# Optimization experiments

Measured on AMD Instinct MI355X. Metric: run time of the kernel, lower is better.

Reference implementation:

```python
import jax, jax.numpy as jnp
import numpy as np

ORDER = 3  # truncation level; num_components = ORDER*(ORDER+1)//2 = 6 (independent weights)


def setup_inputs() -> dict:
    key = jax.random.key(0)
    k1, k2, k3 = jax.random.split(key, 3)
    B, T, D, F = 64, 4096, 128, 64
    C = ORDER * (ORDER + 1) // 2
    sequences = jax.random.normal(k1, (B, T, D), dtype=jnp.float32)
    # ls2t_uniform-style init: scaled uniform per component
    kernel = jax.random.normal(k2, (C, D, F), dtype=jnp.float32) / np.sqrt(D)
    bias = jax.random.normal(k3, (C, F), dtype=jnp.float32) * 0.01
    return {"sequences": sequences, "kernel": kernel, "bias": bias}


def _exclusive_cumsum(x, axis):
    # exclusive cumsum = inclusive cumsum minus self (avoids concat/pad allocs)
    return jnp.cumsum(x, axis=axis) - x


def reference(sequences, kernel, bias):
    # sequences: [B, T, D]; kernel: [C, D, F]; bias: [C, F]
    # M[c] = sequences @ kernel[c] + bias[c]  -> [C, B, T, F]
    M = jnp.einsum('btd,cdf->cbtf', sequences, kernel) + bias[:, None, None, :]
    # Level 1: plain sum over time of first component
    Y = [jnp.sum(M[0], axis=1)]  # [B, F]
    k = 1
    for m in range(1, ORDER):
        R = M[k]
        k += 1
        for _ in range(m):
            # iterated-sum recursion: strictly-lower-triangular (exclusive) cumsum over time
            R = M[k] * _exclusive_cumsum(R, axis=1)
            k += 1
        Y.append(jnp.sum(R, axis=1))
    return jnp.stack(Y, axis=-1)  # [B, F, ORDER]
```

## Files before the change

### kernel.cpp

```cpp
#include <hip/hip_runtime.h>
#include <hip/hip_bf16.h>


#define B_ 64
#define T_ 4096
#define D_ 128
#define F_ 64
#define TB 512
#define TGROUPS (T_ / TB)
#define CHT 16
#define NITER (TB / CHT)
#define TPB 512
#define RING 4

typedef __attribute__((ext_vector_type(8))) short short8v;
typedef __attribute__((ext_vector_type(4))) float f32x4;

__device__ __forceinline__ unsigned short bfb(float x) {
    __hip_bfloat16 h = __float2bfloat16(x);
    unsigned short u;
    __builtin_memcpy(&u, &h, 2);
    return u;
}

#define BAR() asm volatile("s_waitcnt lgkmcnt(0)\n\ts_barrier" ::: "memory")
#define VW(n) asm volatile("s_waitcnt vmcnt(" #n ")" ::: "memory")

__global__ __launch_bounds__(TPB)
void ls2t_kernel(const float* __restrict__ seq,
                 const float* __restrict__ kern,
                 const float* __restrict__ bias,
                 float* __restrict__ ws)
{
    __shared__ float slds[RING][CHT * D_];

    const int tid  = threadIdx.x;
    const int tg   = blockIdx.x;
    const int b    = blockIdx.y;
    const int lane = tid & 63;
    const int w    = tid >> 6;
    const int cg   = w >> 2;
    const int wv   = w & 3;
    const int fr   = lane & 15;
    const int lg   = lane >> 4;
    const int f    = wv * 16 + fr;

    short8v bfrag[3][4];
    float bc[3];
    #pragma unroll
    for (int cc = 0; cc < 3; ++cc) {
        const int c = cg * 3 + cc;
        bc[cc] = bias[c * F_ + f];
        #pragma unroll
        for (int ks = 0; ks < 4; ++ks) {
            const float* kp = kern + ((size_t)c * D_ + ks * 32 + lg * 8) * F_ + f;
            short8v bf;
            #pragma unroll
            for (int j = 0; j < 8; ++j) bf[j] = (short)bfb(kp[(size_t)j * F_]);
            bfrag[cc][ks] = bf;
        }
    }

    const float* sbase = seq + ((size_t)b * T_ + (size_t)tg * TB) * D_;

    const int r_lane = 2 * w + (lane >> 5);
    const int u_lane = lane & 31;
    const int gu     = (u_lane & 24) | ((u_lane ^ r_lane) & 7);
    const float* gsrc0 = sbase
        + ((size_t)((r_lane >> 2) * 128 + (r_lane & 3))) * D_ + gu * 4;

    auto issue = [&](int i, int bufi) {
        const float* src = gsrc0 + (size_t)i * 4 * D_;
        void* dst = (void*)&slds[bufi][w * 256];
        __builtin_amdgcn_global_load_lds(
            (const __attribute__((address_space(1))) void*)src,
            (__attribute__((address_space(3))) void*)dst, 16, 0, 0);
    };

    float x0 = 0.f, x1 = 0.f, x2 = 0.f, x3 = 0.f, x4 = 0.f, x5 = 0.f;

    auto compute = [&](int bufi) {
        const float* L = &slds[bufi][0];
        f32x4 acc[3];
        #pragma unroll
        for (int cc = 0; cc < 3; ++cc)
            acc[cc] = (f32x4){bc[cc], bc[cc], bc[cc], bc[cc]};

        #pragma unroll
        for (int ks = 0; ks < 4; ++ks) {
            const int u0 = ks * 8 + lg * 2;
            const int s0 = (u0 & 24) | ((u0 ^ fr) & 7);
            const int s1 = ((u0 + 1) & 24) | (((u0 + 1) ^ fr) & 7);
            float4 fa = *reinterpret_cast<const float4*>(&L[fr * 128 + s0 * 4]);
            float4 fb = *reinterpret_cast<const float4*>(&L[fr * 128 + s1 * 4]);
            uint4 pk;
            pk.x = __builtin_amdgcn_perm(__float_as_uint(fa.y),
                                         __float_as_uint(fa.x), 0x07060302u);
            pk.y = __builtin_amdgcn_perm(__float_as_uint(fa.w),
                                         __float_as_uint(fa.z), 0x07060302u);
            pk.z = __builtin_amdgcn_perm(__float_as_uint(fb.y),
                                         __float_as_uint(fb.x), 0x07060302u);
            pk.w = __builtin_amdgcn_perm(__float_as_uint(fb.w),
                                         __float_as_uint(fb.z), 0x07060302u);
            short8v a = *reinterpret_cast<short8v*>(&pk);
            #pragma unroll
            for (int cc = 0; cc < 3; ++cc)
                acc[cc] = __builtin_amdgcn_mfma_f32_16x16x32_bf16(
                    a, bfrag[cc][ks], acc[cc], 0, 0, 0);
        }

        #pragma unroll
        for (int r = 0; r < 4; ++r) {
            float p = acc[0][r], q = acc[1][r], rr = acc[2][r];
            x5 = fmaf(rr, x3, x5);
            x4 = fmaf(rr, x1, x4);
            x3 = fmaf(q,  x0, x3);
            x2 += rr;
            x1 += q;
            x0 += p;
        }
    };

    issue(0, 0); issue(1, 1); issue(2, 2);

    #pragma unroll 1
    for (int i = 0; i < NITER - 3; ++i) {
        VW(2);
        BAR();
        issue(i + 3, (i + 3) & 3);
        compute(i & 3);
    }
    VW(2); BAR(); compute(1);
    VW(1); BAR(); compute(2);
    VW(0); BAR(); compute(3);

    #pragma unroll
    for (int m = 16; m <= 32; m <<= 1) {
        float o0 = __shfl_xor(x0, m), o1 = __shfl_xor(x1, m);
        float o2 = __shfl_xor(x2, m), o3 = __shfl_xor(x3, m);
        float o4 = __shfl_xor(x4, m), o5 = __shfl_xor(x5, m);
        const bool up = (lane & m) != 0;
        float A0 = up ? o0 : x0, B0 = up ? x0 : o0;
        float A1 = up ? o1 : x1, B1 = up ? x1 : o1;
        float A2 = up ? o2 : x2, B2 = up ? x2 : o2;
        float A3 = up ? o3 : x3, B3 = up ? x3 : o3;
        float A4 = up ? o4 : x4, B4 = up ? x4 : o4;
        float A5 = up ? o5 : x5, B5 = up ? x5 : o5;
        x5 = A5 + B5 + A3 * B2 + A0 * B4;
        x4 = A4 + B4 + A1 * B2;
        x3 = A3 + B3 + A0 * B1;
        x2 = A2 + B2;
        x1 = A1 + B1;
        x0 = A0 + B0;
    }

    if (lg == 0) {
        float* wp = ws + (((size_t)b * TGROUPS + tg) * F_ + f) * 10;
        if (cg == 0) {
            wp[0] = x0; wp[1] = x1; wp[2] = x2; wp[3] = x4;
        } else {
            wp[4] = x0; wp[5] = x1; wp[6] = x2;
            wp[7] = x3; wp[8] = x4; wp[9] = x5;
        }
    }
}

struct St { float a0, s1, s2, q2, su, sv, sw, qvu, qwv, qwvu; };

__device__ __forceinline__ St mergeSt(const St& A, const St& B) {
    St r;
    r.a0   = A.a0 + B.a0;
    r.q2   = A.q2 + B.q2 + A.s1 * B.s2;
    r.s1   = A.s1 + B.s1;
    r.s2   = A.s2 + B.s2;
    r.qwvu = A.qwvu + B.qwvu + A.qvu * B.sw + A.su * B.qwv;
    r.qwv  = A.qwv + B.qwv + A.sv * B.sw;
    r.qvu  = A.qvu + B.qvu + A.su * B.sv;
    r.su   = A.su + B.su;
    r.sv   = A.sv + B.sv;
    r.sw   = A.sw + B.sw;
    return r;
}

__global__ __launch_bounds__(64)
void ls2t_fold_kernel(const float* __restrict__ ws, float* __restrict__ out)
{
    const int b = blockIdx.x;
    const int f = threadIdx.x;
    St A = {0, 0, 0, 0, 0, 0, 0, 0, 0, 0};
    #pragma unroll
    for (int g = 0; g < TGROUPS; ++g) {
        const float* rp = ws + (((size_t)b * TGROUPS + g) * F_ + f) * 10;
        St r = {rp[0], rp[1], rp[2], rp[3], rp[4],
                rp[5], rp[6], rp[7], rp[8], rp[9]};
        A = mergeSt(A, r);
    }
    float* op = out + ((size_t)b * F_ + f) * 3;
    op[0] = A.a0;
    op[1] = A.q2;
    op[2] = A.qwvu;
}

extern "C" void kernel_launch(void* const* d_in, const int* in_sizes, int n_in,
                              void* d_out, int out_size, void* d_ws, size_t ws_size,
                              hipStream_t stream) {
    const float* seq  = (const float*)d_in[0];
    const float* kern = (const float*)d_in[1];
    const float* bias = (const float*)d_in[2];
    float* out = (float*)d_out;
    float* ws  = (float*)d_ws;

    dim3 g1(TGROUPS, B_);
    ls2t_kernel<<<g1, TPB, 0, stream>>>(seq, kern, bias, ws);
    ls2t_fold_kernel<<<B_, F_, 0, stream>>>(ws, out);
}
```

Before: 43.43 us.

## Replace LDS ring pipeline with direct register double-buffered loads and split blocks

Drops the shared-memory ring filled by global_load_lds and has each lane load its MFMA A-fragment straight from global memory into registers, double-buffered across two chunks. Each component group now gets its own 256-thread block, so the grid doubles and block indices are remapped (presumably to spread work across XCDs). The intent is to remove the LDS round trip and most barriers and to raise occupancy with launch_bounds(256,3). The cost is that both component groups now read the same sequence data separately, doubling global traffic, and the register footprint grows.

```diff
diff --git a/kernel.cpp b/kernel.cpp
--- a/kernel.cpp
+++ b/kernel.cpp
@@ -8,10 +8,9 @@
 #define F_ 64
 #define TB 512
 #define TGROUPS (T_ / TB)
-#define CHT 16
-#define NITER (TB / CHT)
-#define TPB 512
-#define RING 4
+#define NITER 32
+#define TPB 256
+#define NBLK (B_ * TGROUPS * 2)
 
 typedef __attribute__((ext_vector_type(8))) short short8v;
 typedef __attribute__((ext_vector_type(4))) float f32x4;
@@ -23,24 +22,23 @@
     return u;
 }
 
-#define BAR() asm volatile("s_waitcnt lgkmcnt(0)\n\ts_barrier" ::: "memory")
 #define VW(n) asm volatile("s_waitcnt vmcnt(" #n ")" ::: "memory")
 
-__global__ __launch_bounds__(TPB)
+__global__ __launch_bounds__(TPB, 3)
 void ls2t_kernel(const float* __restrict__ seq,
                  const float* __restrict__ kern,
                  const float* __restrict__ bias,
                  float* __restrict__ ws)
 {
-    __shared__ float slds[RING][CHT * D_];
-
-    const int tid  = threadIdx.x;
-    const int tg   = blockIdx.x;
-    const int b    = blockIdx.y;
+    const int tid = threadIdx.x;
+    const int bid     = blockIdx.x;
+    const int logical = (bid & 7) * (NBLK / 8) + (bid >> 3);
+    const int cg = logical & 1;
+    const int tg = (logical >> 1) & (TGROUPS - 1);
+    const int b  = logical >> 4;
+
     const int lane = tid & 63;
-    const int w    = tid >> 6;
-    const int cg   = w >> 2;
-    const int wv   = w & 3;
+    const int wv   = tid >> 6;
     const int fr   = lane & 15;
     const int lg   = lane >> 4;
     const int f    = wv * 16 + fr;
@@ -61,26 +59,22 @@
         }
     }
 
-    const float* sbase = seq + ((size_t)b * T_ + (size_t)tg * TB) * D_;
-
-    const int r_lane = 2 * w + (lane >> 5);
-    const int u_lane = lane & 31;
-    const int gu     = (u_lane & 24) | ((u_lane ^ r_lane) & 7);
-    const float* gsrc0 = sbase
-        + ((size_t)((r_lane >> 2) * 128 + (r_lane & 3))) * D_ + gu * 4;
-
-    auto issue = [&](int i, int bufi) {
-        const float* src = gsrc0 + (size_t)i * 4 * D_;
-        void* dst = (void*)&slds[bufi][w * 256];
-        __builtin_amdgcn_global_load_lds(
-            (const __attribute__((address_space(1))) void*)src,
-            (__attribute__((address_space(3))) void*)dst, 16, 0, 0);
+    const float* gp = seq
+        + ((size_t)b * T_ + (size_t)tg * TB + (fr >> 2) * 128 + (fr & 3)) * D_
+        + lg * 8;
+
+    float4 fA[8], fB[8];
+    auto LD8 = [&](const float* p, float4* A) {
+        const float4* p4 = reinterpret_cast<const float4*>(p);
+        A[0] = p4[0];  A[1] = p4[1];
+        A[2] = p4[8];  A[3] = p4[9];
+        A[4] = p4[16]; A[5] = p4[17];
+        A[6] = p4[24]; A[7] = p4[25];
     };
 
     float x0 = 0.f, x1 = 0.f, x2 = 0.f, x3 = 0.f, x4 = 0.f, x5 = 0.f;
 
-    auto compute = [&](int bufi) {
-        const float* L = &slds[bufi][0];
+    auto compute = [&](const float4* A) {
         f32x4 acc[3];
         #pragma unroll
         for (int cc = 0; cc < 3; ++cc)
@@ -88,20 +82,15 @@
 
         #pragma unroll
         for (int ks = 0; ks < 4; ++ks) {
-            const int u0 = ks * 8 + lg * 2;
-            const int s0 = (u0 & 24) | ((u0 ^ fr) & 7);
-            const int s1 = ((u0 + 1) & 24) | (((u0 + 1) ^ fr) & 7);
-            float4 fa = *reinterpret_cast<const float4*>(&L[fr * 128 + s0 * 4]);
-            float4 fb = *reinterpret_cast<const float4*>(&L[fr * 128 + s1 * 4]);
             uint4 pk;
-            pk.x = __builtin_amdgcn_perm(__float_as_uint(fa.y),
-                                         __float_as_uint(fa.x), 0x07060302u);
-            pk.y = __builtin_amdgcn_perm(__float_as_uint(fa.w),
-                                         __float_as_uint(fa.z), 0x07060302u);
-            pk.z = __builtin_amdgcn_perm(__float_as_uint(fb.y),
-                                         __float_as_uint(fb.x), 0x07060302u);
-            pk.w = __builtin_amdgcn_perm(__float_as_uint(fb.w),
-                                         __float_as_uint(fb.z), 0x07060302u);
+            pk.x = __builtin_amdgcn_perm(__float_as_uint(A[2 * ks].y),
+                                         __float_as_uint(A[2 * ks].x), 0x07060302u);
+            pk.y = __builtin_amdgcn_perm(__float_as_uint(A[2 * ks].w),
+                                         __float_as_uint(A[2 * ks].z), 0x07060302u);
+            pk.z = __builtin_amdgcn_perm(__float_as_uint(A[2 * ks + 1].y),
+                                         __float_as_uint(A[2 * ks + 1].x), 0x07060302u);
+            pk.w = __builtin_amdgcn_perm(__float_as_uint(A[2 * ks + 1].w),
+                                         __float_as_uint(A[2 * ks + 1].z), 0x07060302u);
             short8v a = *reinterpret_cast<short8v*>(&pk);
             #pragma unroll
             for (int cc = 0; cc < 3; ++cc)
@@ -121,18 +110,23 @@
         }
     };
 
-    issue(0, 0); issue(1, 1); issue(2, 2);
+    LD8(gp, fA);
+    LD8(gp + 4 * D_, fB);
+    gp += 8 * D_;
 
     #pragma unroll 1
-    for (int i = 0; i < NITER - 3; ++i) {
-        VW(2);
-        BAR();
-        issue(i + 3, (i + 3) & 3);
-        compute(i & 3);
-    }
-    VW(2); BAR(); compute(1);
-    VW(1); BAR(); compute(2);
-    VW(0); BAR(); compute(3);
+    for (int i = 0; i <= NITER - 4; i += 2) {
+        VW(8);
+        compute(fA);
+        LD8(gp, fA);
+        VW(8);
+        compute(fB);
+        LD8(gp + 4 * D_, fB);
+        gp += 8 * D_;
+        asm volatile("s_barrier");
+    }
+    VW(8); compute(fA);
+    VW(0); compute(fB);
 
     #pragma unroll
     for (int m = 16; m <= 32; m <<= 1) {
@@ -210,7 +204,6 @@
     float* out = (float*)d_out;
     float* ws  = (float*)d_ws;
 
-    dim3 g1(TGROUPS, B_);
-    ls2t_kernel<<<g1, TPB, 0, stream>>>(seq, kern, bias, ws);
+    ls2t_kernel<<<NBLK, TPB, 0, stream>>>(seq, kern, bias, ws);
     ls2t_fold_kernel<<<B_, F_, 0, stream>>>(ws, out);
 }
```

After: 123.7 us. 2.85x slower.
